# Performance work log

Hardware: AMD Instinct MI355X
Metric: run time of the kernel (lower is better)

## Reference

```python
import jax, jax.numpy as jnp
import numpy as np

# Canonical Mamba-1 block dims
D_MODEL = 1024
D_INNER = 2048        # d_model * projection_size (expand=2)
D_STATE = 16          # SSM state size N (Mamba default)
DT_RANK = 64          # d_model // 16 (Mamba default)
KER = 4               # conv_ker
BATCH, SEQ = 2, 1024


def setup_inputs() -> dict:
    key = jax.random.key(0)
    ks = jax.random.split(key, 8)
    sc = lambda k, shape, s: (jax.random.normal(k, shape, dtype=jnp.float32) * s)
    A_log = jnp.log(jnp.broadcast_to(
        jnp.arange(1, D_STATE + 1, dtype=jnp.float32), (D_INNER, D_STATE)))
    return {
        "hidden_states": jax.random.normal(ks[0], (BATCH, SEQ, D_MODEL), dtype=jnp.float32),
        "in_proj_w": sc(ks[1], (D_MODEL, 2 * D_INNER), 0.02),
        "conv_w": sc(ks[2], (D_INNER, 1, KER), 0.1),      # depthwise conv kernel [O, I/groups=1, K]
        "conv_b": jnp.zeros((D_INNER,), dtype=jnp.float32),
        "x_proj_w": sc(ks[3], (D_INNER, DT_RANK + 2 * D_STATE), 0.02),
        "dt_proj_w": sc(ks[4], (DT_RANK, D_INNER), 0.05),
        "dt_proj_b": jnp.full((D_INNER,), -4.6, dtype=jnp.float32),  # softplus(-4.6) ~ 0.01 init dt
        "A_log": A_log,
        "D_skip": jnp.ones((D_INNER,), dtype=jnp.float32),
        "out_proj_w": sc(ks[5], (D_INNER, D_MODEL), 0.02),
    }


def _selective_scan(u, delta, A, Bm, Cm, D_skip):
    """u, delta: [B,L,D]; A: [D,N]; Bm, Cm: [B,L,N]; D_skip: [D]."""
    # Discretize: seq-major for lax.scan
    dA = jnp.exp(jnp.einsum('bld,dn->lbdn', delta, A))            # [L,B,D,N]
    dBu = jnp.einsum('bld,bln,bld->lbdn', delta, Bm, u)           # [L,B,D,N]

    def step(h, ab):
        dA_t, dBu_t = ab
        h = dA_t * h + dBu_t
        return h, h

    h0 = jnp.zeros((u.shape[0], A.shape[0], A.shape[1]), u.dtype)  # [B,D,N]
    _, hs = jax.lax.scan(step, h0, (dA, dBu))                      # hs: [L,B,D,N]
    y = jnp.einsum('lbdn,bln->bld', hs, Cm)
    return y + u * D_skip


def reference(hidden_states, in_proj_w, conv_w, conv_b, x_proj_w,
              dt_proj_w, dt_proj_b, A_log, D_skip, out_proj_w):
    silu = jax.nn.silu
    # Input projection -> (x, res), each [B,L,D_INNER]
    xz = hidden_states @ in_proj_w
    x, res = jnp.split(xz, 2, axis=-1)

    # Causal depthwise conv over sequence: [B,D,L] layout
    x_c = jnp.transpose(x, (0, 2, 1))
    x_c = jax.lax.conv_general_dilated(
        x_c, conv_w, window_strides=(1,), padding=[(KER - 1, 0)],
        dimension_numbers=('NCH', 'OIH', 'NCH'), feature_group_count=D_INNER)
    x_c = x_c + conv_b[None, :, None]
    x = silu(jnp.transpose(x_c, (0, 2, 1)))                        # [B,L,D_INNER]

    # SSM parameterization
    x_dbl = x @ x_proj_w                                           # [B,L,dt_rank+2N]
    dt, Bm, Cm = jnp.split(x_dbl, [DT_RANK, DT_RANK + D_STATE], axis=-1)
    delta = jax.nn.softplus(dt @ dt_proj_w + dt_proj_b)            # [B,L,D_INNER]
    A = -jnp.exp(A_log)                                            # [D_INNER, N]

    y = _selective_scan(x, delta, A, Bm, Cm, D_skip)

    # SiLU gate and output projection
    y = y * silu(res)
    return y @ out_proj_w
```

## Files before the change

### kernel.cpp

```cpp
#include <hip/hip_runtime.h>
#include <hip/hip_bf16.h>
#include <cstdint>

#define D_MODEL  1024
#define D_INNER  2048
#define D_STATE  16
#define DT_RANK  64
#define KERW     4
#define BATCH    2
#define SEQ      1024
#define NTOK     (BATCH * SEQ)
#define CHUNKS   32
#define LOG2C    5
#define LC       (SEQ / CHUNKS)

typedef _Float16 h8 __attribute__((ext_vector_type(8)));
typedef _Float16 h4 __attribute__((ext_vector_type(4)));
typedef float    f32x4 __attribute__((ext_vector_type(4)));

__device__ __forceinline__ float siluf(float x) {
    return x / (1.f + __expf(-x));
}

#define GLOAD_LDS16(g, p) __builtin_amdgcn_global_load_lds( \
    (const __attribute__((address_space(1))) void*)(g),      \
    (__attribute__((address_space(3))) void*)(p), 16, 0, 0)

__global__ __launch_bounds__(256)
void f32_to_f16_k(const float* __restrict__ in, _Float16* __restrict__ out, int n4)
{
    int i = blockIdx.x * 256 + threadIdx.x;
    if (i >= n4) return;
    float4 v = ((const float4*)in)[i];
    h4 h = { (_Float16)v.x, (_Float16)v.y, (_Float16)v.z, (_Float16)v.w };
    *(h4*)(out + (size_t)i * 4) = h;
}

template<int NN>
__global__ __launch_bounds__(256)
void pack_b_f16(const float* __restrict__ B, _Float16* __restrict__ Bp, int K)
{
    constexpr int SH = (NN == 4096) ? 12 : 10;
    int gid = blockIdx.x * 256 + threadIdx.x;
    int n  = gid & (NN - 1);
    int kb = gid >> SH;
    h8 v;
    #pragma unroll
    for (int j = 0; j < 8; ++j)
        v[j] = (_Float16)B[(size_t)(kb * 8 + j) * NN + n];
    *(h8*)(Bp + (size_t)gid * 8) = v;
}

__device__ __forceinline__ void stage_tiles(
    const _Float16* __restrict__ A, const _Float16* __restrict__ Bp,
    _Float16* as, _Float16* bs, int bm, int bn, int k0, int N, int lda, int tid)
{
    #pragma unroll
    for (int i = 0; i < 2; ++i) {
        int c = i * 256 + tid;
        int row = c & 127, kgc = c >> 7;
        const _Float16* g = A + (size_t)(bm + row) * lda + k0 + kgc * 8;
        GLOAD_LDS16(g, as + (size_t)c * 8);
    }
    {
        int c = tid;
        int col = c & 63, kgc = c >> 6;
        const _Float16* g = Bp + ((size_t)((k0 >> 3) + kgc) * N + bn + col) * 8;
        GLOAD_LDS16(g, bs + (size_t)c * 8);
    }
}

__global__ __launch_bounds__(256)
void gemm_f16_mfma(const _Float16* __restrict__ A, const _Float16* __restrict__ Bp,
                   float* __restrict__ C, int M, int N, int K, int lda, int ldc)
{
    __shared__ alignas(16) _Float16 As[2][4 * 128 * 8];
    __shared__ alignas(16) _Float16 Bs[2][4 * 64 * 8];

    const int tid = threadIdx.x;
    const int l = tid & 63, w = tid >> 6;
    const int wm = w >> 1, wn = w & 1;

    const int nwg = gridDim.x;
    const int qch = nwg >> 3;
    const int wg  = ((blockIdx.x & 7) * qch) + (blockIdx.x >> 3);
    const int nbn = N >> 6;
    const int bn  = (wg % nbn) * 64;
    const int bm  = (wg / nbn) * 128;

    const int kslice = K / gridDim.z;
    const int kbeg = blockIdx.z * kslice;
    const int kend = kbeg + kslice;

    f32x4 acc[4][2] = {};
    const int kg = l >> 4, r = l & 15;

    stage_tiles(A, Bp, As[0], Bs[0], bm, bn, kbeg, N, lda, tid);
    __syncthreads();

    int cur = 0;
    for (int k0 = kbeg; k0 < kend; k0 += 32) {
        if (k0 + 32 < kend)
            stage_tiles(A, Bp, As[cur ^ 1], Bs[cur ^ 1], bm, bn, k0 + 32, N, lda, tid);

        h8 a[4], b[2];
        #pragma unroll
        for (int mi = 0; mi < 4; ++mi)
            a[mi] = *(const h8*)(As[cur] + (size_t)(kg * 128 + wm * 64 + mi * 16 + r) * 8);
        #pragma unroll
        for (int ni = 0; ni < 2; ++ni)
            b[ni] = *(const h8*)(Bs[cur] + (size_t)(kg * 64 + wn * 32 + ni * 16 + r) * 8);

        #pragma unroll
        for (int mi = 0; mi < 4; ++mi)
            #pragma unroll
            for (int ni = 0; ni < 2; ++ni)
                acc[mi][ni] = __builtin_amdgcn_mfma_f32_16x16x32_f16(
                    a[mi], b[ni], acc[mi][ni], 0, 0, 0);

        __syncthreads();
        cur ^= 1;
    }

    float* dst = C + (size_t)blockIdx.z * M * ldc;
    const int q = l >> 4;
    #pragma unroll
    for (int mi = 0; mi < 4; ++mi)
        #pragma unroll
        for (int ni = 0; ni < 2; ++ni)
            #pragma unroll
            for (int j = 0; j < 4; ++j)
                dst[(size_t)(bm + wm * 64 + mi * 16 + q * 4 + j) * ldc
                    + (bn + wn * 32 + ni * 16 + r)] = acc[mi][ni][j];
}

template<bool BIAS, bool SOFTPLUS>
__global__ __launch_bounds__(256)
void gemm_f32(const float* __restrict__ A, const float* __restrict__ B,
              const float* __restrict__ bias, float* __restrict__ C,
              int M, int N, int K, int lda, int ldb, int ldc)
{
    __shared__ float As[16][68];
    __shared__ float Bs[16][68];
    const int tid = threadIdx.x;
    const int tx = tid & 15, ty = tid >> 4;
    const int bm = blockIdx.y * 64, bn = blockIdx.x * 64;

    float acc[4][4] = {};

    const int ar  = tid >> 2;
    const int ac4 = (tid & 3) << 2;
    const int bkr = tid >> 4;
    const int bc4 = (tid & 15) << 2;

    for (int k0 = 0; k0 < K; k0 += 16) {
        float4 av = make_float4(0.f, 0.f, 0.f, 0.f);
        {
            int row = bm + ar;
            if (row < M)
                av = *(const float4*)(A + (size_t)row * lda + (k0 + ac4));
        }
        As[ac4 + 0][ar] = av.x; As[ac4 + 1][ar] = av.y;
        As[ac4 + 2][ar] = av.z; As[ac4 + 3][ar] = av.w;

        float4 bv = make_float4(0.f, 0.f, 0.f, 0.f);
        {
            int col = bn + bc4;
            const float* bp = B + (size_t)(k0 + bkr) * ldb + col;
            if (col + 3 < N) {
                bv = *(const float4*)bp;
            } else {
                if (col + 0 < N) bv.x = bp[0];
                if (col + 1 < N) bv.y = bp[1];
                if (col + 2 < N) bv.z = bp[2];
                if (col + 3 < N) bv.w = bp[3];
            }
        }
        Bs[bkr][bc4 + 0] = bv.x; Bs[bkr][bc4 + 1] = bv.y;
        Bs[bkr][bc4 + 2] = bv.z; Bs[bkr][bc4 + 3] = bv.w;

        __syncthreads();

        #pragma unroll
        for (int kk = 0; kk < 16; ++kk) {
            float a[4], b[4];
            #pragma unroll
            for (int i = 0; i < 4; ++i) a[i] = As[kk][ty * 4 + i];
            #pragma unroll
            for (int j = 0; j < 4; ++j) b[j] = Bs[kk][tx * 4 + j];
            #pragma unroll
            for (int i = 0; i < 4; ++i)
                #pragma unroll
                for (int j = 0; j < 4; ++j)
                    acc[i][j] = fmaf(a[i], b[j], acc[i][j]);
        }
        __syncthreads();
    }

    #pragma unroll
    for (int i = 0; i < 4; ++i) {
        int row = bm + ty * 4 + i;
        if (row >= M) continue;
        #pragma unroll
        for (int j = 0; j < 4; ++j) {
            int col = bn + tx * 4 + j;
            if (col >= N) continue;
            float v = acc[i][j];
            if (BIAS) v += bias[col];
            if (SOFTPLUS) v = (v > 20.f) ? v : log1pf(__expf(v));
            C[(size_t)row * ldc + col] = v;
        }
    }
}

__global__ __launch_bounds__(256)
void gemm_f32_splitk(const float* __restrict__ A, const float* __restrict__ B,
                     float* __restrict__ part,
                     int M, int N, int K, int lda, int ldb, int ldc)
{
    __shared__ float As[16][68];
    __shared__ float Bs[16][68];
    const int tid = threadIdx.x;
    const int tx = tid & 15, ty = tid >> 4;
    const int bm = blockIdx.y * 64, bn = blockIdx.x * 64;
    const int kslice = K / gridDim.z;
    const int kbeg = blockIdx.z * kslice;

    float acc[4][4] = {};

    const int ar  = tid >> 2;
    const int ac4 = (tid & 3) << 2;
    const int bkr = tid >> 4;
    const int bc4 = (tid & 15) << 2;

    for (int k0 = kbeg; k0 < kbeg + kslice; k0 += 16) {
        float4 av;
        {
            int row = bm + ar;
            av = *(const float4*)(A + (size_t)row * lda + (k0 + ac4));
        }
        As[ac4 + 0][ar] = av.x; As[ac4 + 1][ar] = av.y;
        As[ac4 + 2][ar] = av.z; As[ac4 + 3][ar] = av.w;

        float4 bv = make_float4(0.f, 0.f, 0.f, 0.f);
        {
            int col = bn + bc4;
            const float* bp = B + (size_t)(k0 + bkr) * ldb + col;
            if (col + 3 < N) {
                bv = *(const float4*)bp;
            } else {
                if (col + 0 < N) bv.x = bp[0];
                if (col + 1 < N) bv.y = bp[1];
                if (col + 2 < N) bv.z = bp[2];
                if (col + 3 < N) bv.w = bp[3];
            }
        }
        Bs[bkr][bc4 + 0] = bv.x; Bs[bkr][bc4 + 1] = bv.y;
        Bs[bkr][bc4 + 2] = bv.z; Bs[bkr][bc4 + 3] = bv.w;

        __syncthreads();

        #pragma unroll
        for (int kk = 0; kk < 16; ++kk) {
            float a[4], b[4];
            #pragma unroll
            for (int i = 0; i < 4; ++i) a[i] = As[kk][ty * 4 + i];
            #pragma unroll
            for (int j = 0; j < 4; ++j) b[j] = Bs[kk][tx * 4 + j];
            #pragma unroll
            for (int i = 0; i < 4; ++i)
                #pragma unroll
                for (int j = 0; j < 4; ++j)
                    acc[i][j] = fmaf(a[i], b[j], acc[i][j]);
        }
        __syncthreads();
    }

    float* dst = part + (size_t)blockIdx.z * M * ldc;
    #pragma unroll
    for (int i = 0; i < 4; ++i) {
        int row = bm + ty * 4 + i;
        #pragma unroll
        for (int j = 0; j < 4; ++j) {
            int col = bn + tx * 4 + j;
            if (col >= N) continue;
            dst[(size_t)row * ldc + col] = acc[i][j];
        }
    }
}

__global__ __launch_bounds__(256)
void reduce_splitk(const float* __restrict__ part, float* __restrict__ out,
                   int n, int S)
{
    int i = blockIdx.x * 256 + threadIdx.x;
    if (i >= n) return;
    float s = 0.f;
    for (int j = 0; j < S; ++j) s += part[(size_t)j * n + i];
    out[i] = s;
}

__global__ __launch_bounds__(256)
void conv_silu(const float* __restrict__ xz, const float* __restrict__ conv_w,
               const float* __restrict__ conv_b, float* __restrict__ u)
{
    int idx = blockIdx.x * 256 + threadIdx.x;
    if (idx >= NTOK * D_INNER) return;
    int d = idx & (D_INNER - 1);
    int t = idx >> 11;
    int l = t & (SEQ - 1);
    int b = t >> 10;

    float w0 = conv_w[d * 4 + 0], w1 = conv_w[d * 4 + 1];
    float w2 = conv_w[d * 4 + 2], w3 = conv_w[d * 4 + 3];

    const float* base = xz + (size_t)b * SEQ * (2 * D_INNER) + d;
    float acc = conv_b[d];
    if (l >= 3) acc += w0 * base[(size_t)(l - 3) * (2 * D_INNER)];
    if (l >= 2) acc += w1 * base[(size_t)(l - 2) * (2 * D_INNER)];
    if (l >= 1) acc += w2 * base[(size_t)(l - 1) * (2 * D_INNER)];
    acc += w3 * base[(size_t)l * (2 * D_INNER)];

    u[idx] = siluf(acc);
}

__global__ __launch_bounds__(256)
void scan_pass1(const float* __restrict__ delta, const float* __restrict__ u,
                const float* __restrict__ xdbl, const float* __restrict__ A_log,
                float* __restrict__ Aprod, float* __restrict__ Hend)
{
    int t = blockIdx.x * 256 + threadIdx.x;
    if (t >= BATCH * CHUNKS * D_INNER) return;
    int d  = t & (D_INNER - 1);
    int bc = t >> 11;
    int c  = bc & (CHUNKS - 1);
    int b  = bc >> LOG2C;

    float An[16];
    {
        const float4* a4 = (const float4*)(A_log + d * 16);
        #pragma unroll
        for (int q = 0; q < 4; ++q) {
            float4 v = a4[q];
            An[q * 4 + 0] = -__expf(v.x);
            An[q * 4 + 1] = -__expf(v.y);
            An[q * 4 + 2] = -__expf(v.z);
            An[q * 4 + 3] = -__expf(v.w);
        }
    }

    const float* dp = delta + ((size_t)b * SEQ + c * LC) * D_INNER + d;
    const float* up = u     + ((size_t)b * SEQ + c * LC) * D_INNER + d;
    const float* xb = xdbl  + ((size_t)b * SEQ + c * LC) * 96 + DT_RANK;

    float h[16], ap[16];
    #pragma unroll
    for (int n = 0; n < 16; ++n) { h[n] = 0.f; ap[n] = 1.f; }

    #pragma unroll 2
    for (int l = 0; l < LC; ++l) {
        float dt = dp[(size_t)l * D_INNER];
        float ut = up[(size_t)l * D_INNER];
        const float4* b4 = (const float4*)(xb + l * 96);
        float4 B0 = b4[0], B1 = b4[1], B2 = b4[2], B3 = b4[3];
        float Bv[16] = { B0.x, B0.y, B0.z, B0.w, B1.x, B1.y, B1.z, B1.w,
                         B2.x, B2.y, B2.z, B2.w, B3.x, B3.y, B3.z, B3.w };
        float dtu = dt * ut;
        #pragma unroll
        for (int n = 0; n < 16; ++n) {
            float da = __expf(dt * An[n]);
            h[n]  = fmaf(da, h[n], dtu * Bv[n]);
            ap[n] *= da;
        }
    }

    float4* hp = (float4*)(Hend  + (size_t)t * 16);
    float4* pp = (float4*)(Aprod + (size_t)t * 16);
    #pragma unroll
    for (int q = 0; q < 4; ++q) {
        hp[q] = make_float4(h[q*4+0], h[q*4+1], h[q*4+2], h[q*4+3]);
        pp[q] = make_float4(ap[q*4+0], ap[q*4+1], ap[q*4+2], ap[q*4+3]);
    }
}

__global__ __launch_bounds__(256)
void scan_pass2(const float* __restrict__ Aprod, float* __restrict__ HendHin)
{
    int idx = blockIdx.x * 256 + threadIdx.x;
    if (idx >= BATCH * D_INNER * D_STATE) return;
    int n = idx & 15;
    int d = (idx >> 4) & (D_INNER - 1);
    int b = idx >> 15;

    float h = 0.f;
    for (int c = 0; c < CHUNKS; ++c) {
        size_t j = ((((size_t)b * CHUNKS + c) * D_INNER) + d) * 16 + n;
        float ap = Aprod[j];
        float he = HendHin[j];
        HendHin[j] = h;
        h = ap * h + he;
    }
}

__global__ __launch_bounds__(256)
void scan_pass3(const float* __restrict__ delta, const float* __restrict__ u,
                const float* __restrict__ xdbl, const float* __restrict__ xz,
                const float* __restrict__ A_log, const float* __restrict__ D_skip,
                const float* __restrict__ Hin, _Float16* __restrict__ ygh)
{
    int t = blockIdx.x * 256 + threadIdx.x;
    if (t >= BATCH * CHUNKS * D_INNER) return;
    int d  = t & (D_INNER - 1);
    int bc = t >> 11;
    int c  = bc & (CHUNKS - 1);
    int b  = bc >> LOG2C;

    float An[16];
    {
        const float4* a4 = (const float4*)(A_log + d * 16);
        #pragma unroll
        for (int q = 0; q < 4; ++q) {
            float4 v = a4[q];
            An[q * 4 + 0] = -__expf(v.x);
            An[q * 4 + 1] = -__expf(v.y);
            An[q * 4 + 2] = -__expf(v.z);
            An[q * 4 + 3] = -__expf(v.w);
        }
    }
    float Dd = D_skip[d];

    float h[16];
    {
        const float4* h4p = (const float4*)(Hin + (size_t)t * 16);
        #pragma unroll
        for (int q = 0; q < 4; ++q) {
            float4 v = h4p[q];
            h[q * 4 + 0] = v.x; h[q * 4 + 1] = v.y;
            h[q * 4 + 2] = v.z; h[q * 4 + 3] = v.w;
        }
    }

    const float* dp = delta + ((size_t)b * SEQ + c * LC) * D_INNER + d;
    const float* up = u     + ((size_t)b * SEQ + c * LC) * D_INNER + d;
    const float* xb = xdbl  + ((size_t)b * SEQ + c * LC) * 96 + DT_RANK;
    const float* rp = xz    + ((size_t)b * SEQ + c * LC) * (2 * D_INNER) + D_INNER + d;
    _Float16*    yp = ygh   + ((size_t)b * SEQ + c * LC) * 8192 + d;

    #pragma unroll 2
    for (int l = 0; l < LC; ++l) {
        float dt = dp[(size_t)l * D_INNER];
        float ut = up[(size_t)l * D_INNER];
        float res = rp[(size_t)l * (2 * D_INNER)];
        const float4* b4 = (const float4*)(xb + l * 96);
        float4 B0 = b4[0], B1 = b4[1], B2 = b4[2], B3 = b4[3];
        float4 C0 = b4[4], C1 = b4[5], C2 = b4[6], C3 = b4[7];
        float Bv[16] = { B0.x, B0.y, B0.z, B0.w, B1.x, B1.y, B1.z, B1.w,
                         B2.x, B2.y, B2.z, B2.w, B3.x, B3.y, B3.z, B3.w };
        float Cv[16] = { C0.x, C0.y, C0.z, C0.w, C1.x, C1.y, C1.z, C1.w,
                         C2.x, C2.y, C2.z, C2.w, C3.x, C3.y, C3.z, C3.w };
        float dtu = dt * ut;
        float y = 0.f;
        #pragma unroll
        for (int n = 0; n < 16; ++n) {
            float da = __expf(dt * An[n]);
            h[n] = fmaf(da, h[n], dtu * Bv[n]);
            y = fmaf(h[n], Cv[n], y);
        }
        yp[(size_t)l * 8192] = (_Float16)((y + ut * Dd) * siluf(res));
    }
}

extern "C" void kernel_launch(void* const* d_in, const int* in_sizes, int n_in,
                              void* d_out, int out_size, void* d_ws, size_t ws_size,
                              hipStream_t stream)
{
    const float* H      = (const float*)d_in[0];
    const float* Win    = (const float*)d_in[1];
    const float* convw  = (const float*)d_in[2];
    const float* convb  = (const float*)d_in[3];
    const float* xprojw = (const float*)d_in[4];
    const float* dtw    = (const float*)d_in[5];
    const float* dtb    = (const float*)d_in[6];
    const float* Alog   = (const float*)d_in[7];
    const float* Dskip  = (const float*)d_in[8];
    const float* Wout   = (const float*)d_in[9];
    float* out = (float*)d_out;

    float* ws    = (float*)d_ws;
    float* xz    = ws;
    float* u     = xz   + (size_t)NTOK * 4096;
    float* xdbl  = u    + (size_t)NTOK * 2048;
    float* delta = xdbl + (size_t)NTOK * 96;
    float* Aprod = delta + (size_t)NTOK * 2048;
    float* Hend  = Aprod + (size_t)BATCH * CHUNKS * D_INNER * 16;

    _Float16* Hh    = (_Float16*)delta;
    _Float16* Winp  = (_Float16*)delta + 2 * 1024 * 1024;
    float*    part  = delta;
    float*    part4 = delta;
    _Float16* ygh   = (_Float16*)xz;
    _Float16* Woutp = (_Float16*)Aprod;

    dim3 blk(256);

    f32_to_f16_k<<<(NTOK * D_MODEL / 4) / 256, blk, 0, stream>>>(H, Hh, NTOK * D_MODEL / 4);
    pack_b_f16<4096><<<((D_MODEL / 8) * 4096) / 256, blk, 0, stream>>>(Win, Winp, D_MODEL);

    gemm_f16_mfma<<<dim3((4096 / 64) * (NTOK / 128), 1, 1), blk, 0, stream>>>(
        Hh, Winp, xz, NTOK, 2 * D_INNER, D_MODEL, D_MODEL, 2 * D_INNER);

    conv_silu<<<(NTOK * D_INNER) / 256, blk, 0, stream>>>(xz, convw, convb, u);

    gemm_f32_splitk<<<dim3(2, NTOK / 64, 16), blk, 0, stream>>>(
        u, xprojw, part, NTOK, 96, D_INNER, D_INNER, 96, 96);
    reduce_splitk<<<(NTOK * 96 + 255) / 256, blk, 0, stream>>>(
        part, xdbl, NTOK * 96, 16);

    gemm_f32<true, true><<<dim3(D_INNER / 64, NTOK / 64), blk, 0, stream>>>(
        xdbl, dtw, dtb, delta, NTOK, D_INNER, DT_RANK, 96, D_INNER, D_INNER);

    {
        int nthr = BATCH * CHUNKS * D_INNER;
        scan_pass1<<<nthr / 256, blk, 0, stream>>>(delta, u, xdbl, Alog, Aprod, Hend);
        scan_pass2<<<(BATCH * D_INNER * 16) / 256, blk, 0, stream>>>(Aprod, Hend);
        scan_pass3<<<nthr / 256, blk, 0, stream>>>(delta, u, xdbl, xz, Alog, Dskip,
                                                   Hend , ygh);
    }

    pack_b_f16<1024><<<((D_INNER / 8) * 1024) / 256, blk, 0, stream>>>(Wout, Woutp, D_INNER);

    gemm_f16_mfma<<<dim3((1024 / 64) * (NTOK / 128), 1, 2), blk, 0, stream>>>(
        ygh, Woutp, part4, NTOK, D_MODEL, D_INNER, 8192, D_MODEL);
    reduce_splitk<<<(NTOK * D_MODEL) / 256, blk, 0, stream>>>(
        part4, out, NTOK * D_MODEL, 2);
}
```

Measured before the change: 340.3 us.

## Split scan state across two lanes per channel with software-prefetched loads

Scan passes 1 and 3 now give each channel two threads, each holding 8 of the 16 state entries. The two partial outputs are combined with a cross-half wave shuffle, and only one lane writes. The per-step loads of delta, u, B/C and res are software-pipelined one step ahead. This doubles thread count and cuts registers per thread to raise occupancy and hide latency, at the cost of duplicated delta/u/res loads and an extra shuffle per step.

```diff
diff --git a/kernel.cpp b/kernel.cpp
--- a/kernel.cpp
+++ b/kernel.cpp
@@ -329,18 +329,21 @@
                 const float* __restrict__ xdbl, const float* __restrict__ A_log,
                 float* __restrict__ Aprod, float* __restrict__ Hend)
 {
-    int t = blockIdx.x * 256 + threadIdx.x;
-    if (t >= BATCH * CHUNKS * D_INNER) return;
-    int d  = t & (D_INNER - 1);
-    int bc = t >> 11;
-    int c  = bc & (CHUNKS - 1);
-    int b  = bc >> LOG2C;
-
-    float An[16];
+    int gid = blockIdx.x * 256 + threadIdx.x;
+    if (gid >= BATCH * CHUNKS * D_INNER * 2) return;
+    int lane = gid & 63;
+    int wv   = gid >> 6;
+    int dsub = lane & 31, nh = lane >> 5;
+    int dblk = wv & 63;
+    int c    = (wv >> 6) & (CHUNKS - 1);
+    int b    = wv >> (6 + LOG2C);
+    int d    = dblk * 32 + dsub;
+
+    float An[8];
     {
-        const float4* a4 = (const float4*)(A_log + d * 16);
-        #pragma unroll
-        for (int q = 0; q < 4; ++q) {
+        const float4* a4 = (const float4*)(A_log + d * 16 + nh * 8);
+        #pragma unroll
+        for (int q = 0; q < 2; ++q) {
             float4 v = a4[q];
             An[q * 4 + 0] = -__expf(v.x);
             An[q * 4 + 1] = -__expf(v.y);
@@ -351,36 +354,48 @@
 
     const float* dp = delta + ((size_t)b * SEQ + c * LC) * D_INNER + d;
     const float* up = u     + ((size_t)b * SEQ + c * LC) * D_INNER + d;
-    const float* xb = xdbl  + ((size_t)b * SEQ + c * LC) * 96 + DT_RANK;
-
-    float h[16], ap[16];
+    const float* xb = xdbl  + ((size_t)b * SEQ + c * LC) * 96 + DT_RANK + nh * 8;
+
+    float h[8], ap[8];
     #pragma unroll
-    for (int n = 0; n < 16; ++n) { h[n] = 0.f; ap[n] = 1.f; }
-
-    #pragma unroll 2
-    for (int l = 0; l < LC; ++l) {
-        float dt = dp[(size_t)l * D_INNER];
-        float ut = up[(size_t)l * D_INNER];
-        const float4* b4 = (const float4*)(xb + l * 96);
-        float4 B0 = b4[0], B1 = b4[1], B2 = b4[2], B3 = b4[3];
-        float Bv[16] = { B0.x, B0.y, B0.z, B0.w, B1.x, B1.y, B1.z, B1.w,
-                         B2.x, B2.y, B2.z, B2.w, B3.x, B3.y, B3.z, B3.w };
+    for (int n = 0; n < 8; ++n) { h[n] = 0.f; ap[n] = 1.f; }
+
+    float  dt = dp[0], ut = up[0];
+    float4 Bq0 = *(const float4*)(xb);
+    float4 Bq1 = *(const float4*)(xb + 4);
+
+    for (int l = 0; l < LC - 1; ++l) {
+        float  dt_n = dp[(size_t)(l + 1) * D_INNER];
+        float  ut_n = up[(size_t)(l + 1) * D_INNER];
+        float4 B0n  = *(const float4*)(xb + (l + 1) * 96);
+        float4 B1n  = *(const float4*)(xb + (l + 1) * 96 + 4);
+
+        float Bv[8] = { Bq0.x, Bq0.y, Bq0.z, Bq0.w, Bq1.x, Bq1.y, Bq1.z, Bq1.w };
         float dtu = dt * ut;
         #pragma unroll
-        for (int n = 0; n < 16; ++n) {
+        for (int n = 0; n < 8; ++n) {
             float da = __expf(dt * An[n]);
             h[n]  = fmaf(da, h[n], dtu * Bv[n]);
             ap[n] *= da;
         }
-    }
-
-    float4* hp = (float4*)(Hend  + (size_t)t * 16);
-    float4* pp = (float4*)(Aprod + (size_t)t * 16);
-    #pragma unroll
-    for (int q = 0; q < 4; ++q) {
-        hp[q] = make_float4(h[q*4+0], h[q*4+1], h[q*4+2], h[q*4+3]);
-        pp[q] = make_float4(ap[q*4+0], ap[q*4+1], ap[q*4+2], ap[q*4+3]);
-    }
+        dt = dt_n; ut = ut_n; Bq0 = B0n; Bq1 = B1n;
+    }
+    {
+        float Bv[8] = { Bq0.x, Bq0.y, Bq0.z, Bq0.w, Bq1.x, Bq1.y, Bq1.z, Bq1.w };
+        float dtu = dt * ut;
+        #pragma unroll
+        for (int n = 0; n < 8; ++n) {
+            float da = __expf(dt * An[n]);
+            h[n]  = fmaf(da, h[n], dtu * Bv[n]);
+            ap[n] *= da;
+        }
+    }
+
+    size_t off = ((((size_t)b * CHUNKS + c) * D_INNER) + d) * 16 + nh * 8;
+    *(float4*)(Hend  + off)     = make_float4(h[0], h[1], h[2], h[3]);
+    *(float4*)(Hend  + off + 4) = make_float4(h[4], h[5], h[6], h[7]);
+    *(float4*)(Aprod + off)     = make_float4(ap[0], ap[1], ap[2], ap[3]);
+    *(float4*)(Aprod + off + 4) = make_float4(ap[4], ap[5], ap[6], ap[7]);
 }
 
 __global__ __launch_bounds__(256)
@@ -408,18 +423,21 @@
                 const float* __restrict__ A_log, const float* __restrict__ D_skip,
                 const float* __restrict__ Hin, _Float16* __restrict__ ygh)
 {
-    int t = blockIdx.x * 256 + threadIdx.x;
-    if (t >= BATCH * CHUNKS * D_INNER) return;
-    int d  = t & (D_INNER - 1);
-    int bc = t >> 11;
-    int c  = bc & (CHUNKS - 1);
-    int b  = bc >> LOG2C;
-
-    float An[16];
+    int gid = blockIdx.x * 256 + threadIdx.x;
+    if (gid >= BATCH * CHUNKS * D_INNER * 2) return;
+    int lane = gid & 63;
+    int wv   = gid >> 6;
+    int dsub = lane & 31, nh = lane >> 5;
+    int dblk = wv & 63;
+    int c    = (wv >> 6) & (CHUNKS - 1);
+    int b    = wv >> (6 + LOG2C);
+    int d    = dblk * 32 + dsub;
+
+    float An[8];
     {
-        const float4* a4 = (const float4*)(A_log + d * 16);
-        #pragma unroll
-        for (int q = 0; q < 4; ++q) {
+        const float4* a4 = (const float4*)(A_log + d * 16 + nh * 8);
+        #pragma unroll
+        for (int q = 0; q < 2; ++q) {
             float4 v = a4[q];
             An[q * 4 + 0] = -__expf(v.x);
             An[q * 4 + 1] = -__expf(v.y);
@@ -429,44 +447,56 @@
     }
     float Dd = D_skip[d];
 
-    float h[16];
+    float h[8];
     {
-        const float4* h4p = (const float4*)(Hin + (size_t)t * 16);
-        #pragma unroll
-        for (int q = 0; q < 4; ++q) {
-            float4 v = h4p[q];
-            h[q * 4 + 0] = v.x; h[q * 4 + 1] = v.y;
-            h[q * 4 + 2] = v.z; h[q * 4 + 3] = v.w;
-        }
+        size_t off = ((((size_t)b * CHUNKS + c) * D_INNER) + d) * 16 + nh * 8;
+        float4 v0 = *(const float4*)(Hin + off);
+        float4 v1 = *(const float4*)(Hin + off + 4);
+        h[0] = v0.x; h[1] = v0.y; h[2] = v0.z; h[3] = v0.w;
+        h[4] = v1.x; h[5] = v1.y; h[6] = v1.z; h[7] = v1.w;
     }
 
     const float* dp = delta + ((size_t)b * SEQ + c * LC) * D_INNER + d;
     const float* up = u     + ((size_t)b * SEQ + c * LC) * D_INNER + d;
-    const float* xb = xdbl  + ((size_t)b * SEQ + c * LC) * 96 + DT_RANK;
+    const float* xb = xdbl  + ((size_t)b * SEQ + c * LC) * 96 + DT_RANK + nh * 8;
     const float* rp = xz    + ((size_t)b * SEQ + c * LC) * (2 * D_INNER) + D_INNER + d;
     _Float16*    yp = ygh   + ((size_t)b * SEQ + c * LC) * 8192 + d;
 
-    #pragma unroll 2
+    float  dt = dp[0], ut = up[0], res = rp[0];
+    float4 Bq0 = *(const float4*)(xb);
+    float4 Bq1 = *(const float4*)(xb + 4);
+    float4 Cq0 = *(const float4*)(xb + 16);
+    float4 Cq1 = *(const float4*)(xb + 20);
+
     for (int l = 0; l < LC; ++l) {
-        float dt = dp[(size_t)l * D_INNER];
-        float ut = up[(size_t)l * D_INNER];
-        float res = rp[(size_t)l * (2 * D_INNER)];
-        const float4* b4 = (const float4*)(xb + l * 96);
-        float4 B0 = b4[0], B1 = b4[1], B2 = b4[2], B3 = b4[3];
-        float4 C0 = b4[4], C1 = b4[5], C2 = b4[6], C3 = b4[7];
-        float Bv[16] = { B0.x, B0.y, B0.z, B0.w, B1.x, B1.y, B1.z, B1.w,
-                         B2.x, B2.y, B2.z, B2.w, B3.x, B3.y, B3.z, B3.w };
-        float Cv[16] = { C0.x, C0.y, C0.z, C0.w, C1.x, C1.y, C1.z, C1.w,
-                         C2.x, C2.y, C2.z, C2.w, C3.x, C3.y, C3.z, C3.w };
+        float dt_n, ut_n, res_n;
+        float4 B0n, B1n, C0n, C1n;
+        if (l + 1 < LC) {
+            dt_n  = dp[(size_t)(l + 1) * D_INNER];
+            ut_n  = up[(size_t)(l + 1) * D_INNER];
+            res_n = rp[(size_t)(l + 1) * (2 * D_INNER)];
+            B0n = *(const float4*)(xb + (l + 1) * 96);
+            B1n = *(const float4*)(xb + (l + 1) * 96 + 4);
+            C0n = *(const float4*)(xb + (l + 1) * 96 + 16);
+            C1n = *(const float4*)(xb + (l + 1) * 96 + 20);
+        }
+
+        float Bv[8] = { Bq0.x, Bq0.y, Bq0.z, Bq0.w, Bq1.x, Bq1.y, Bq1.z, Bq1.w };
+        float Cv[8] = { Cq0.x, Cq0.y, Cq0.z, Cq0.w, Cq1.x, Cq1.y, Cq1.z, Cq1.w };
         float dtu = dt * ut;
         float y = 0.f;
         #pragma unroll
-        for (int n = 0; n < 16; ++n) {
+        for (int n = 0; n < 8; ++n) {
             float da = __expf(dt * An[n]);
             h[n] = fmaf(da, h[n], dtu * Bv[n]);
             y = fmaf(h[n], Cv[n], y);
         }
-        yp[(size_t)l * 8192] = (_Float16)((y + ut * Dd) * siluf(res));
+        y += __shfl_xor(y, 32, 64);
+        if (nh == 0)
+            yp[(size_t)l * 8192] = (_Float16)((y + ut * Dd) * siluf(res));
+
+        dt = dt_n; ut = ut_n; res = res_n;
+        Bq0 = B0n; Bq1 = B1n; Cq0 = C0n; Cq1 = C1n;
     }
 }
 
@@ -520,11 +550,11 @@
         xdbl, dtw, dtb, delta, NTOK, D_INNER, DT_RANK, 96, D_INNER, D_INNER);
 
     {
-        int nthr = BATCH * CHUNKS * D_INNER;
-        scan_pass1<<<nthr / 256, blk, 0, stream>>>(delta, u, xdbl, Alog, Aprod, Hend);
+        int nthr2 = BATCH * CHUNKS * D_INNER * 2;
+        scan_pass1<<<nthr2 / 256, blk, 0, stream>>>(delta, u, xdbl, Alog, Aprod, Hend);
         scan_pass2<<<(BATCH * D_INNER * 16) / 256, blk, 0, stream>>>(Aprod, Hend);
-        scan_pass3<<<nthr / 256, blk, 0, stream>>>(delta, u, xdbl, xz, Alog, Dskip,
-                                                   Hend , ygh);
+        scan_pass3<<<nthr2 / 256, blk, 0, stream>>>(delta, u, xdbl, xz, Alog, Dskip,
+                                                    Hend , ygh);
     }
 
     pack_b_f16<1024><<<((D_INNER / 8) * 1024) / 256, blk, 0, stream>>>(Wout, Woutp, D_INNER);
```

Measured after the change: 290.8 us. -14.5%, faster.
